# Optimization experiments

Measured on AMD Instinct MI355X. Metric: run time of the kernel, lower is better.

Reference implementation:

```python
import jax, jax.numpy as jnp
import numpy as np

DIM = 2048
DIM_HEADS = 64
NUM_HEADS = DIM // DIM_HEADS  # 32


def setup_inputs() -> dict:
    key = jax.random.key(0)
    k1, k2, k3, k4 = jax.random.split(key, 4)
    B, N = 2, 2048
    x = jax.random.normal(k1, (B, N, DIM), dtype=jnp.float32)
    freqs = jax.random.normal(k2, (N, DIM_HEADS), dtype=jnp.float32)
    W_qkv = jax.random.normal(k3, (3 * DIM, DIM), dtype=jnp.float32) * 0.02
    W_out = jax.random.normal(k4, (DIM, DIM), dtype=jnp.float32) * 0.02
    return {"x": x, "freqs": freqs, "W_qkv": W_qkv, "W_out": W_out}


def _rotate_half(x):
    # split last dim into two halves (j=2), return cat(-x2, x1)
    x1, x2 = jnp.split(x, 2, axis=-1)
    return jnp.concatenate([-x2, x1], axis=-1)


def _apply_rotary_pos_emb(t, freqs, scale=1.0):
    # t: [b, h, n, d]; freqs: [n, rot_dim]; rotary math in float32
    out_dtype = t.dtype
    rot_dim = freqs.shape[-1]
    seq_len = t.shape[-2]
    freqs = freqs.astype(jnp.float32)[-seq_len:, :]  # [n, rot_dim]
    t = t.astype(jnp.float32)
    t_rot, t_unrot = t[..., :rot_dim], t[..., rot_dim:]
    t_rot = t_rot * jnp.cos(freqs) * scale + _rotate_half(t_rot) * jnp.sin(freqs) * scale
    return jnp.concatenate([t_rot.astype(out_dtype), t_unrot.astype(out_dtype)], axis=-1)


def reference(x, freqs, W_qkv, W_out):
    B, N, _ = x.shape
    h, d = NUM_HEADS, DIM_HEADS
    # fused QKV projection (Linear, no bias): x @ W_qkv.T
    qkv = jnp.einsum('bnc,fc->bnf', x, W_qkv)  # [B, N, 3*DIM]
    q, k, v = jnp.split(qkv, 3, axis=-1)
    q = q.reshape(B, N, h, d).transpose(0, 2, 1, 3)  # [B, h, N, d]
    k = k.reshape(B, N, h, d).transpose(0, 2, 1, 3)
    v = v.reshape(B, N, h, d).transpose(0, 2, 1, 3)
    # equal q/k seq lens -> ratio = 1, same freqs for both
    q = _apply_rotary_pos_emb(q, freqs)
    k = _apply_rotary_pos_emb(k, freqs)
    # scaled dot-product attention (non-causal)
    scale = 1.0 / np.sqrt(d).astype(np.float32)
    scores = jnp.einsum('bhqd,bhkd->bhqk', q, k) * scale
    attn = jax.nn.softmax(scores, axis=-1)
    out = jnp.einsum('bhqk,bhkd->bhqd', attn, v)
    out = out.transpose(0, 2, 1, 3).reshape(B, N, h * d)  # [B, N, DIM]
    return jnp.einsum('bnc,oc->bno', out, W_out)
```

## Files before the change

### kernel.cpp

```cpp
#include <hip/hip_runtime.h>

#define DIMC 2048
#define NSEQ 2048
#define NBATCH 2
#define NH 32
#define DH 64
#define BHEADS (NBATCH*NH)
#define MROWS (NBATCH*NSEQ)
#define NQKV (3*DIMC)

typedef __attribute__((ext_vector_type(8))) short short8;
typedef __attribute__((ext_vector_type(4))) float f32x4;
typedef __attribute__((ext_vector_type(4))) unsigned int uint4v;
typedef __attribute__((ext_vector_type(2))) unsigned int u32x2;

static __device__ __forceinline__ unsigned short f2bf(float f) {
  union { float f; unsigned int u; } v; v.f = f;
  unsigned int r = (v.u + 0x7FFFu + ((v.u >> 16) & 1u)) >> 16;
  return (unsigned short)r;
}

static __device__ __forceinline__ unsigned int cvt_pk_bf16(float lo, float hi) {
  unsigned int r;
  asm("v_cvt_pk_bf16_f32 %0, %1, %2" : "=v"(r) : "v"(lo), "v"(hi));
  return r;
}

#define BAR()    __builtin_amdgcn_s_barrier()
#define FENCE()  asm volatile("" ::: "memory")
#define LGKM0()  asm volatile("s_waitcnt lgkmcnt(0)" ::: "memory")
#define LGKM8()  asm volatile("s_waitcnt lgkmcnt(8)" ::: "memory")
#define VM(n)    asm volatile("s_waitcnt vmcnt(" #n ")" ::: "memory")

__global__ __launch_bounds__(256) void cvt_bf16(const float* __restrict__ in,
                                                unsigned short* __restrict__ out,
                                                int n8) {
  int i = blockIdx.x * blockDim.x + threadIdx.x;
  int stride = gridDim.x * blockDim.x;
  for (; i < n8; i += stride) {
    const float4* p = (const float4*)in + (size_t)i * 2;
    float4 a = p[0], b = p[1];
    union { unsigned short u[8]; uint4v v; } o;
    o.u[0] = f2bf(a.x); o.u[1] = f2bf(a.y); o.u[2] = f2bf(a.z); o.u[3] = f2bf(a.w);
    o.u[4] = f2bf(b.x); o.u[5] = f2bf(b.y); o.u[6] = f2bf(b.z); o.u[7] = f2bf(b.w);
    *((uint4v*)out + i) = o.v;
  }
}

__global__ __launch_bounds__(256) void build_cs(const float* __restrict__ freqs,
                                                float2* __restrict__ cs, int n) {
  int i = blockIdx.x * blockDim.x + threadIdx.x;
  if (i < n) { float f = freqs[i]; cs[i] = make_float2(cosf(f), sinf(f)); }
}

#define QSCALE 0.18033688011112042f
#define SLOT 24576

template<int EPI>
__global__ __launch_bounds__(512, 1) void gemm128(
    const unsigned short* __restrict__ A,
    const unsigned short* __restrict__ Bm,
    int Kdim, int Ncols,
    float* __restrict__ Cout,
    unsigned short* __restrict__ qo, unsigned short* __restrict__ ko,
    unsigned short* __restrict__ vo, const float2* __restrict__ cs)
{
  extern __shared__ char Lds[];
  const int t = threadIdx.x;
  const int w = t >> 6, lane = t & 63, lr = lane & 15, g = lane >> 4;
  const int wm = w >> 2, wn = w & 3;
  const int gxs = (g * 16) ^ (((lr >> 1) & 3) << 4);

  const int nx = gridDim.x;
  int orig = blockIdx.y * nx + blockIdx.x;
  int cpx = (nx * gridDim.y) >> 3;
  int id = (orig & 7) * cpx + (orig >> 3);
  const int m0 = (id / nx) * 128;
  const int n0 = (id % nx) * 256;

  const int rowt = t >> 2;
  const int colt = (((t & 3) ^ ((t >> 3) & 3))) * 8;
  const unsigned short* Abase = A + (size_t)(m0 + rowt) * Kdim + colt;
  const unsigned short* Bbase = Bm + (size_t)(n0 + rowt) * Kdim + colt;
  char* dstw = Lds + w * 1024;

  auto STAGE = [&](int sbuf, int T) {
    const unsigned short* sa = Abase + T * 32;
    const unsigned short* sb = Bbase + T * 32;
    __builtin_amdgcn_global_load_lds(
        (const __attribute__((address_space(1))) void*)sa,
        (__attribute__((address_space(3))) void*)(dstw + sbuf), 16, 0, 0);
    __builtin_amdgcn_global_load_lds(
        (const __attribute__((address_space(1))) void*)sb,
        (__attribute__((address_space(3))) void*)(dstw + sbuf + 8192), 16, 0, 0);
    __builtin_amdgcn_global_load_lds(
        (const __attribute__((address_space(1))) void*)(sb + (size_t)128 * Kdim),
        (__attribute__((address_space(3))) void*)(dstw + sbuf + 16384), 16, 0, 0);
  };

  short8 AfE[4], BfE[4], AfO[4], BfO[4];
  auto LDAB = [&](short8 (&Af)[4], short8 (&Bf)[4], int rb) {
    const char* ap = Lds + rb + (wm * 64 + lr) * 64 + gxs;
    const char* bp = Lds + rb + 8192 + (wn * 64 + lr) * 64 + gxs;
    #pragma unroll
    for (int m = 0; m < 4; m++) Af[m] = *(const short8*)(ap + m * 1024);
    #pragma unroll
    for (int n = 0; n < 4; n++) Bf[n] = *(const short8*)(bp + n * 1024);
  };

  f32x4 acc[4][4];
  f32x4 zero = {0.0f, 0.0f, 0.0f, 0.0f};
  #pragma unroll
  for (int i = 0; i < 4; i++)
    #pragma unroll
    for (int j = 0; j < 4; j++) acc[i][j] = zero;

  auto MM = [&](short8 (&Af)[4], short8 (&Bf)[4]) {
    __builtin_amdgcn_s_setprio(1);
    #pragma unroll
    for (int m = 0; m < 4; m++)
      #pragma unroll
      for (int n = 0; n < 4; n++)
        acc[m][n] = __builtin_amdgcn_mfma_f32_16x16x32_bf16(Af[m], Bf[n], acc[m][n], 0, 0, 0);
    __builtin_amdgcn_s_setprio(0);
  };

  const int NT = Kdim >> 5;

  STAGE(0, 0); STAGE(SLOT, 1);
  VM(3);
  BAR(); FENCE();
  LDAB(AfE, BfE, 0);
  STAGE(2 * SLOT, 2);
  VM(3);
  BAR(); FENCE();

  int rs = SLOT;
  int ss = 3 * SLOT;
  for (int i = 0; i < NT; i += 2) {
    if (i + 1 < NT) LDAB(AfO, BfO, rs);
    if (i + 3 < NT) STAGE(ss, i + 3);
    if (i + 1 < NT) { LGKM8(); } else { LGKM0(); }
    MM(AfE, BfE);
    if (i + 3 < NT) { VM(3); } else if (i + 2 < NT) { VM(0); }
    BAR(); FENCE();
    rs += SLOT; if (rs == 4 * SLOT) rs = 0;
    ss += SLOT; if (ss == 4 * SLOT) ss = 0;
    if (i + 2 < NT) LDAB(AfE, BfE, rs);
    if (i + 4 < NT) STAGE(ss, i + 4);
    if (i + 2 < NT) { LGKM8(); } else { LGKM0(); }
    MM(AfO, BfO);
    if (i + 4 < NT) { VM(3); } else if (i + 3 < NT) { VM(0); }
    BAR(); FENCE();
    rs += SLOT; if (rs == 4 * SLOT) rs = 0;
    ss += SLOT; if (ss == 4 * SLOT) ss = 0;
  }

  if (EPI == 0) {
    #pragma unroll
    for (int m = 0; m < 4; m++) {
      #pragma unroll
      for (int r = 0; r < 4; r++) {
        int row = m0 + wm * 64 + m * 16 + g * 4 + r;
        #pragma unroll
        for (int n = 0; n < 4; n++)
          Cout[(size_t)row * Ncols + (n0 + wn * 64 + n * 16 + lr)] = acc[m][n][r];
      }
    }
  } else {
    const int which = n0 >> 11;
    const int head = ((n0 & 2047) + wn * 64) >> 6;
    #pragma unroll
    for (int m = 0; m < 4; m++) {
      #pragma unroll
      for (int r = 0; r < 4; r++) {
        int row = m0 + wm * 64 + m * 16 + g * 4 + r;
        int b = row >> 11, ntok = row & 2047;
        size_t obase = ((size_t)(b * NH + head) * NSEQ + ntok) * DH;
        #pragma unroll
        for (int n = 0; n < 4; n++) {
          int d = n * 16 + lr;
          float val = acc[m][n][r];
          if (which == 2) {
            vo[obase + d] = f2bf(val);
          } else {
            float other = acc[m][n ^ 2][r];
            float2 c2 = cs[ntok * DH + d];
            float rot = (d < 32) ? (val * c2.x - other * c2.y)
                                 : (val * c2.x + other * c2.y);
            if (which == 0) qo[obase + d] = f2bf(rot * QSCALE);
            else            ko[obase + d] = f2bf(rot);
          }
        }
      }
    }
  }
}

__global__ __launch_bounds__(256, 4) void attn_fa(
    const unsigned short* __restrict__ qb,
    const unsigned short* __restrict__ kb,
    const unsigned short* __restrict__ vb,
    unsigned short* __restrict__ aob)
{
  __shared__ __align__(16) unsigned short Kl[64 * 64];
  __shared__ __align__(16) unsigned short Vt[64 * 72];
  __shared__ __align__(16) unsigned short Pl[4][32 * 76];

  const int t = threadIdx.x;
  const int w = t >> 6, lane = t & 63, lr = lane & 15, g = lane >> 4;
  const int bh = blockIdx.y;
  const int q0 = blockIdx.x * 128 + w * 32;
  const size_t hbase = (size_t)bh * NSEQ * DH;

  short8 qf[2][2];
  #pragma unroll
  for (int qt = 0; qt < 2; qt++)
    #pragma unroll
    for (int hf = 0; hf < 2; hf++)
      qf[qt][hf] = *(const short8*)(qb + hbase + (size_t)(q0 + qt * 16 + lr) * DH + hf * 32 + g * 8);

  f32x4 zero = {0.0f, 0.0f, 0.0f, 0.0f};
  f32x4 oacc[2][4];
  #pragma unroll
  for (int qt = 0; qt < 2; qt++)
    #pragma unroll
    for (int dv = 0; dv < 4; dv++) oacc[qt][dv] = zero;
  float mrun[2] = {-1e30f, -1e30f};
  float lrun[2] = {0.0f, 0.0f};

  int kro[2], kdo_[2];
  #pragma unroll
  for (int c = 0; c < 2; c++) {
    int b = w * 2048 + c * 1024 + lane * 16;
    int row = b >> 7;
    int off = b ^ ((row & 7) << 4);
    kro[c] = row;
    kdo_[c] = (off >> 1) & 63;
  }
  const int vr0 = (t & 31) * 2;
  const int vhv = (t >> 5) * 8;

  unsigned short* prow0 = &Pl[w][lr * 76];
  unsigned short* prow1 = &Pl[w][(16 + lr) * 76];

  for (int kv0 = 0; kv0 < NSEQ; kv0 += 64) {
    __syncthreads();
    #pragma unroll
    for (int c = 0; c < 2; c++) {
      const unsigned short* src = kb + hbase + (size_t)(kv0 + kro[c]) * DH + kdo_[c];
      __builtin_amdgcn_global_load_lds(
          (const __attribute__((address_space(1))) void*)src,
          (__attribute__((address_space(3))) void*)(Kl + w * 1024 + c * 512), 16, 0, 0);
    }
    {
      const unsigned short* s0 = vb + hbase + (size_t)(kv0 + vr0) * DH + vhv;
      short8 v0 = *(const short8*)(s0);
      short8 v1 = *(const short8*)(s0 + DH);
      #pragma unroll
      for (int j = 0; j < 8; j++) {
        unsigned int p = ((unsigned short)v0[j]) | (((unsigned int)(unsigned short)v1[j]) << 16);
        *(unsigned int*)&Vt[(vhv + j) * 72 + vr0] = p;
      }
    }
    __syncthreads();

    f32x4 s[2][4];
    #pragma unroll
    for (int kt = 0; kt < 4; kt++) {
      int row = kt * 16 + lr;
      int sw = (row & 7) << 4;
      int byteA = (row * 128 + g * 16) ^ sw;
      int byteB = (row * 128 + 64 + g * 16) ^ sw;
      short8 kA = *(const short8*)((const char*)Kl + byteA);
      short8 kB = *(const short8*)((const char*)Kl + byteB);
      #pragma unroll
      for (int qt = 0; qt < 2; qt++) {
        f32x4 a0 = __builtin_amdgcn_mfma_f32_16x16x32_bf16(kA, qf[qt][0], zero, 0, 0, 0);
        s[qt][kt] = __builtin_amdgcn_mfma_f32_16x16x32_bf16(kB, qf[qt][1], a0, 0, 0, 0);
      }
    }

    float nm[2];
    #pragma unroll
    for (int qt = 0; qt < 2; qt++) {
      f32x4 m01 = s[qt][0];
      #pragma unroll
      for (int kt = 1; kt < 4; kt++) {
        f32x4 sv = s[qt][kt];
        m01[0] = fmaxf(m01[0], sv[0]); m01[1] = fmaxf(m01[1], sv[1]);
        m01[2] = fmaxf(m01[2], sv[2]); m01[3] = fmaxf(m01[3], sv[3]);
      }
      float v = fmaxf(fmaxf(m01[0], m01[1]), fmaxf(m01[2], m01[3]));
      v = fmaxf(v, __shfl_xor(v, 16));
      v = fmaxf(v, __shfl_xor(v, 32));
      nm[qt] = v;
    }

    if (!__all(fmaxf(nm[0] - mrun[0], nm[1] - mrun[1]) <= 8.0f)) {
      const int sb = (lane & 48) + ((lane & 48) >> 2);
      #pragma unroll
      for (int qt = 0; qt < 2; qt++) {
        float m2 = fmaxf(mrun[qt], nm[qt]);
        float cc = exp2f(mrun[qt] - m2);
        mrun[qt] = m2;
        lrun[qt] *= cc;
        float c0r = __shfl(cc, sb + 0);
        float c1r = __shfl(cc, sb + 1);
        float c2r = __shfl(cc, sb + 2);
        float c3r = __shfl(cc, sb + 3);
        #pragma unroll
        for (int dv = 0; dv < 4; dv++) {
          f32x4 a = oacc[qt][dv];
          a[0] *= c0r; a[1] *= c1r; a[2] *= c2r; a[3] *= c3r;
          oacc[qt][dv] = a;
        }
      }
    }

    #pragma unroll
    for (int qt = 0; qt < 2; qt++) {
      float mq = mrun[qt];
      float ls = 0.0f;
      unsigned short* prow = qt ? prow1 : prow0;
      #pragma unroll
      for (int kt = 0; kt < 4; kt++) {
        f32x4 sv = s[qt][kt];
        float p0 = exp2f(sv[0] - mq), p1 = exp2f(sv[1] - mq);
        float p2 = exp2f(sv[2] - mq), p3 = exp2f(sv[3] - mq);
        ls += (p0 + p1) + (p2 + p3);
        u32x2 uu;
        uu.x = cvt_pk_bf16(p0, p1);
        uu.y = cvt_pk_bf16(p2, p3);
        *(u32x2*)(prow + kt * 16 + g * 4) = uu;
      }
      ls += __shfl_xor(ls, 16);
      ls += __shfl_xor(ls, 32);
      lrun[qt] += ls;
    }

    #pragma unroll
    for (int c0 = 0; c0 < 2; c0++) {
      short8 pa0 = *(const short8*)(prow0 + c0 * 32 + g * 8);
      short8 pa1 = *(const short8*)(prow1 + c0 * 32 + g * 8);
      #pragma unroll
      for (int dv = 0; dv < 4; dv++) {
        short8 vf = *(const short8*)&Vt[(dv * 16 + lr) * 72 + c0 * 32 + g * 8];
        oacc[0][dv] = __builtin_amdgcn_mfma_f32_16x16x32_bf16(pa0, vf, oacc[0][dv], 0, 0, 0);
        oacc[1][dv] = __builtin_amdgcn_mfma_f32_16x16x32_bf16(pa1, vf, oacc[1][dv], 0, 0, 0);
      }
    }
  }

  const int b = bh >> 5, h = bh & 31;
  const int sb = (lane & 48) + ((lane & 48) >> 2);
  #pragma unroll
  for (int qt = 0; qt < 2; qt++) {
    float inv = 1.0f / lrun[qt];
    float ir[4];
    ir[0] = __shfl(inv, sb + 0);
    ir[1] = __shfl(inv, sb + 1);
    ir[2] = __shfl(inv, sb + 2);
    ir[3] = __shfl(inv, sb + 3);
    #pragma unroll
    for (int r = 0; r < 4; r++) {
      int ntok = q0 + qt * 16 + g * 4 + r;
      size_t ob = ((size_t)(b * NSEQ + ntok)) * DIMC + h * DH;
      #pragma unroll
      for (int dv = 0; dv < 4; dv++)
        aob[ob + dv * 16 + lr] = f2bf(oacc[qt][dv][r] * ir[r]);
    }
  }
}

extern "C" void kernel_launch(void* const* d_in, const int* in_sizes, int n_in,
                              void* d_out, int out_size, void* d_ws, size_t ws_size,
                              hipStream_t stream) {
  const float* x     = (const float*)d_in[0];
  const float* freqs = (const float*)d_in[1];
  const float* Wqkv  = (const float*)d_in[2];
  const float* Wout  = (const float*)d_in[3];
  float* out = (float*)d_out;

  char* ws = (char*)d_ws;
  size_t off = 0;
  auto alloc = [&](size_t bytes) {
    void* p = ws + off;
    off += (bytes + 255) & ~(size_t)255;
    return p;
  };
  unsigned short* xb    = (unsigned short*)alloc((size_t)MROWS * DIMC * 2);
  unsigned short* wqkvb = (unsigned short*)alloc((size_t)NQKV * DIMC * 2);
  unsigned short* woutb = (unsigned short*)alloc((size_t)DIMC * DIMC * 2);
  unsigned short* qbuf  = (unsigned short*)alloc((size_t)BHEADS * NSEQ * DH * 2);
  unsigned short* kbuf  = (unsigned short*)alloc((size_t)BHEADS * NSEQ * DH * 2);
  unsigned short* vbuf  = (unsigned short*)alloc((size_t)BHEADS * NSEQ * DH * 2);
  float2* cst           = (float2*)alloc((size_t)NSEQ * DH * sizeof(float2));
  unsigned short* aob   = xb;

  (void)hipFuncSetAttribute((const void*)gemm128<1>,
      hipFuncAttributeMaxDynamicSharedMemorySize, 4 * SLOT);
  (void)hipFuncSetAttribute((const void*)gemm128<0>,
      hipFuncAttributeMaxDynamicSharedMemorySize, 4 * SLOT);

  cvt_bf16<<<2048, 256, 0, stream>>>(x, xb, MROWS * DIMC / 8);
  cvt_bf16<<<2048, 256, 0, stream>>>(Wqkv, wqkvb, NQKV * DIMC / 8);
  cvt_bf16<<<1024, 256, 0, stream>>>(Wout, woutb, DIMC * DIMC / 8);
  build_cs<<<(NSEQ * DH + 255) / 256, 256, 0, stream>>>(freqs, cst, NSEQ * DH);

  gemm128<1><<<dim3(NQKV / 256, MROWS / 128), 512, 4 * SLOT, stream>>>(
      xb, wqkvb, DIMC, NQKV, nullptr, qbuf, kbuf, vbuf, cst);

  attn_fa<<<dim3(NSEQ / 128, BHEADS), 256, 0, stream>>>(qbuf, kbuf, vbuf, aob);

  gemm128<0><<<dim3(DIMC / 256, MROWS / 128), 512, 4 * SLOT, stream>>>(
      aob, woutb, DIMC, DIMC, out, nullptr, nullptr, nullptr, nullptr);
}
```

Before: 374.8 us.

## Use three-slot LDS ring in GEMM to allow two blocks per CU

Shrinks the GEMM shared-memory ring buffer from four slots to three and sets launch bounds to two blocks per CU. The aim is to raise occupancy so two workgroups can overlap each other's memory latency. Prefetch depth drops from three stages ahead to two, and every iteration now waits for all outstanding global loads (vmcnt 0) before the barrier. The tighter register budget may also cause spills.

```diff
diff --git a/kernel.cpp b/kernel.cpp
--- a/kernel.cpp
+++ b/kernel.cpp
@@ -57,7 +57,7 @@
 #define SLOT 24576
 
 template<int EPI>
-__global__ __launch_bounds__(512, 1) void gemm128(
+__global__ __launch_bounds__(512, 2) void gemm128(
     const unsigned short* __restrict__ A,
     const unsigned short* __restrict__ Bm,
     int Kdim, int Ncols,
@@ -127,33 +127,31 @@
 
   const int NT = Kdim >> 5;
 
-  STAGE(0, 0); STAGE(SLOT, 1);
-  VM(3);
+  STAGE(0, 0);
+  VM(0);
   BAR(); FENCE();
   LDAB(AfE, BfE, 0);
-  STAGE(2 * SLOT, 2);
-  VM(3);
+  STAGE(SLOT, 1);
+  VM(0);
   BAR(); FENCE();
 
-  int rs = SLOT;
-  int ss = 3 * SLOT;
+  int s_rd = SLOT;
+  int s_st = 2 * SLOT;
   for (int i = 0; i < NT; i += 2) {
-    if (i + 1 < NT) LDAB(AfO, BfO, rs);
-    if (i + 3 < NT) STAGE(ss, i + 3);
-    if (i + 1 < NT) { LGKM8(); } else { LGKM0(); }
+    if (i + 2 < NT) STAGE(s_st, i + 2);
+    if (i + 1 < NT) { LDAB(AfO, BfO, s_rd); LGKM8(); } else { LGKM0(); }
     MM(AfE, BfE);
-    if (i + 3 < NT) { VM(3); } else if (i + 2 < NT) { VM(0); }
+    VM(0);
     BAR(); FENCE();
-    rs += SLOT; if (rs == 4 * SLOT) rs = 0;
-    ss += SLOT; if (ss == 4 * SLOT) ss = 0;
-    if (i + 2 < NT) LDAB(AfE, BfE, rs);
-    if (i + 4 < NT) STAGE(ss, i + 4);
-    if (i + 2 < NT) { LGKM8(); } else { LGKM0(); }
+    s_rd += SLOT; if (s_rd == 3 * SLOT) s_rd = 0;
+    s_st += SLOT; if (s_st == 3 * SLOT) s_st = 0;
+    if (i + 3 < NT) STAGE(s_st, i + 3);
+    if (i + 2 < NT) { LDAB(AfE, BfE, s_rd); LGKM8(); } else { LGKM0(); }
     MM(AfO, BfO);
-    if (i + 4 < NT) { VM(3); } else if (i + 3 < NT) { VM(0); }
+    VM(0);
     BAR(); FENCE();
-    rs += SLOT; if (rs == 4 * SLOT) rs = 0;
-    ss += SLOT; if (ss == 4 * SLOT) ss = 0;
+    s_rd += SLOT; if (s_rd == 3 * SLOT) s_rd = 0;
+    s_st += SLOT; if (s_st == 3 * SLOT) s_st = 0;
   }
 
   if (EPI == 0) {
@@ -399,20 +397,20 @@
   unsigned short* aob   = xb;
 
   (void)hipFuncSetAttribute((const void*)gemm128<1>,
-      hipFuncAttributeMaxDynamicSharedMemorySize, 4 * SLOT);
+      hipFuncAttributeMaxDynamicSharedMemorySize, 3 * SLOT);
   (void)hipFuncSetAttribute((const void*)gemm128<0>,
-      hipFuncAttributeMaxDynamicSharedMemorySize, 4 * SLOT);
+      hipFuncAttributeMaxDynamicSharedMemorySize, 3 * SLOT);
 
   cvt_bf16<<<2048, 256, 0, stream>>>(x, xb, MROWS * DIMC / 8);
   cvt_bf16<<<2048, 256, 0, stream>>>(Wqkv, wqkvb, NQKV * DIMC / 8);
   cvt_bf16<<<1024, 256, 0, stream>>>(Wout, woutb, DIMC * DIMC / 8);
   build_cs<<<(NSEQ * DH + 255) / 256, 256, 0, stream>>>(freqs, cst, NSEQ * DH);
 
-  gemm128<1><<<dim3(NQKV / 256, MROWS / 128), 512, 4 * SLOT, stream>>>(
+  gemm128<1><<<dim3(NQKV / 256, MROWS / 128), 512, 3 * SLOT, stream>>>(
       xb, wqkvb, DIMC, NQKV, nullptr, qbuf, kbuf, vbuf, cst);
 
   attn_fa<<<dim3(NSEQ / 128, BHEADS), 256, 0, stream>>>(qbuf, kbuf, vbuf, aob);
 
-  gemm128<0><<<dim3(DIMC / 256, MROWS / 128), 512, 4 * SLOT, stream>>>(
+  gemm128<0><<<dim3(DIMC / 256, MROWS / 128), 512, 3 * SLOT, stream>>>(
       aob, woutb, DIMC, DIMC, out, nullptr, nullptr, nullptr, nullptr);
 }
```

Result: slower. 404.0 us (+7.8%).
